# Optimization experiments

Hardware: AMD Instinct MI355X
Metric: run time of the kernel (lower is better)

The kernel has to match this reference:

```python
import jax, jax.numpy as jnp
import numpy as np

N_HEADS = 16

@jax.checkpoint
def feature_fn(x, neurons, weights):
    # x [B,S,D], neurons [N,D,R], weights [B,S,N] -> h [B,S,R]
    all_h = jnp.einsum('bsd,ndr->bsnr', x, neurons)
    return jnp.einsum('bsnr,bsn->bsr', all_h, weights)

@jax.checkpoint
def restore_fn(h, neurons, weights):
    # h [B,S,R], neurons [N,R,D], weights [B,S,N] -> out [B,S,D]
    all_out = jnp.einsum('bsr,nrd->bsnd', h, neurons)
    return jnp.einsum('bsnd,bsn->bsd', all_out, weights)


def setup_inputs() -> dict:
    key = jax.random.key(0)
    ks = jax.random.split(key, 12)
    B, S, D, R, N = 2, 2048, 1024, 128, 8
    inp = {
        'x': jax.random.normal(ks[0], (B, S, D), jnp.float32),
        'f_qk_neurons': jax.random.normal(ks[1], (N, D, R), jnp.float32) * 0.02,
        'f_v_neurons': jax.random.normal(ks[2], (N, D, R), jnp.float32) * 0.02,
        'r_qk_neurons': jax.random.normal(ks[3], (N, R, D), jnp.float32) * 0.02,
        'r_v_neurons': jax.random.normal(ks[4], (N, R, D), jnp.float32) * 0.02,
        'fqk_weights_Q': jax.random.uniform(ks[5], (B, S, N), jnp.float32),
        'fqk_weights_K': jax.random.uniform(ks[6], (B, S, N), jnp.float32),
        'fv_weights': jax.random.uniform(ks[7], (B, S, N), jnp.float32),
        'rqk_weights_Q': jax.random.uniform(ks[8], (B, S, N), jnp.float32),
        'rqk_weights_K': jax.random.uniform(ks[9], (B, S, N), jnp.float32),
        'rv_weights': jax.random.uniform(ks[10], (B, S, N), jnp.float32),
        'W_O': jax.random.normal(ks[11], (D, D), jnp.float32) * 0.02,
    }
    return inp


def reference(x, f_qk_neurons, f_v_neurons, r_qk_neurons, r_v_neurons,
              fqk_weights_Q, fqk_weights_K, fv_weights,
              rqk_weights_Q, rqk_weights_K, rv_weights, W_O):
    B, S, D = x.shape
    H = N_HEADS
    d_head = D // H
    # neuron-mixture feature projections (shared QK pool)
    h_q = feature_fn(x, f_qk_neurons, fqk_weights_Q)
    h_k = feature_fn(x, f_qk_neurons, fqk_weights_K)
    h_v = feature_fn(x, f_v_neurons, fv_weights)
    # neuron-mixture restore projections
    Q = restore_fn(h_q, r_qk_neurons, rqk_weights_Q)
    K = restore_fn(h_k, r_qk_neurons, rqk_weights_K)
    V = restore_fn(h_v, r_v_neurons, rv_weights)
    # split heads: [B,S,D] -> [B,H,S,d_head]
    Q = Q.reshape(B, S, H, d_head).transpose(0, 2, 1, 3)
    K = K.reshape(B, S, H, d_head).transpose(0, 2, 1, 3)
    V = V.reshape(B, S, H, d_head).transpose(0, 2, 1, 3)
    scale = jnp.sqrt(jnp.float32(d_head))
    scores = jnp.einsum('bhsd,bhtd->bhst', Q, K) / scale
    causal_mask = jnp.tril(jnp.ones((S, S), dtype=jnp.bool_))
    scores = jnp.where(causal_mask, scores, jnp.finfo(scores.dtype).min)
    attn = jax.nn.softmax(scores, axis=-1)
    attn_out = jnp.einsum('bhst,bhtd->bhsd', attn, V)
    attn_out = attn_out.transpose(0, 2, 1, 3).reshape(B, S, D)
    return attn_out @ W_O
```

## Files before the change

### kernel.cpp

```cpp
#include <hip/hip_runtime.h>
#include <stdint.h>

typedef __attribute__((ext_vector_type(8))) __bf16 bf16x8;
typedef __attribute__((ext_vector_type(4))) float f32x4;
typedef __attribute__((ext_vector_type(4))) unsigned short us4;
typedef __attribute__((ext_vector_type(8))) unsigned short us8v;

__device__ __forceinline__ unsigned short f2b(float f){
  unsigned int u = __builtin_bit_cast(unsigned int, f);
  unsigned int r = (u + 0x7fffu + ((u >> 16) & 1u)) >> 16;
  return (unsigned short)r;
}
__device__ __forceinline__ unsigned short f2b_fast(float f){
  unsigned int u = __builtin_bit_cast(unsigned int, f);
  return (unsigned short)((u + 0x8000u) >> 16);
}
__device__ __forceinline__ float b2f(unsigned short h){
  unsigned int u = ((unsigned int)h) << 16;
  return __builtin_bit_cast(float, u);
}

#define KDIM 1024

__global__ __launch_bounds__(256) void k_prep(
    const float* __restrict__ x,   unsigned short* __restrict__ Xbf,
    const float* __restrict__ fqk, unsigned short* __restrict__ FqkT,
    const float* __restrict__ fv,  unsigned short* __restrict__ FvT,
    const float* __restrict__ rqk, unsigned short* __restrict__ RqkT,
    const float* __restrict__ rv,  unsigned short* __restrict__ RvT,
    const float* __restrict__ wo,  unsigned short* __restrict__ WOT)
{
  __shared__ float tile[32][33];
  int blk = blockIdx.x;
  int tid = threadIdx.x;
  if (blk < 4096){
    int idx = blk * 256 + tid;
    float4 v = ((const float4*)x)[idx];
    us4 o; o.x = f2b(v.x); o.y = f2b(v.y); o.z = f2b(v.z); o.w = f2b(v.w);
    ((us4*)Xbf)[idx] = o;
    return;
  }
  int t = blk - 4096;
  int mid = t >> 10;
  int within = t & 1023;
  const float* src; unsigned short* dst;
  int b, R, C, tr, tc;
  if (mid < 2){
    src = mid == 0 ? fqk : fv;  dst = mid == 0 ? FqkT : FvT;
    R = 1024; C = 128;
    b = within >> 7; int tw = within & 127; tr = tw >> 2; tc = tw & 3;
  } else {
    src = mid == 2 ? rqk : (mid == 3 ? rv : wo);
    dst = mid == 2 ? RqkT : (mid == 3 ? RvT : WOT);
    R = 1024; C = 1024;
    b = 0; tr = within >> 5; tc = within & 31;
  }
  int r = tid >> 3, c0 = (tid & 7) * 4;
  size_t base = (size_t)b * R * C;
  float4 v = *(const float4*)&src[base + (size_t)(tr*32 + r) * C + tc*32 + c0];
  tile[r][c0+0] = v.x; tile[r][c0+1] = v.y; tile[r][c0+2] = v.z; tile[r][c0+3] = v.w;
  __syncthreads();
  us4 o;
  o.x = f2b(tile[c0+0][r]); o.y = f2b(tile[c0+1][r]);
  o.z = f2b(tile[c0+2][r]); o.w = f2b(tile[c0+3][r]);
  *(us4*)&dst[base + (size_t)(tc*32 + r) * R + tr*32 + c0] = o;
}

__global__ __launch_bounds__(256) void k_mix(const unsigned short* __restrict__ AH,
    const float* __restrict__ fwq, const float* __restrict__ fwk, const float* __restrict__ fwv,
    const float* __restrict__ rwq, const float* __restrict__ rwk, const float* __restrict__ rwv,
    unsigned short* __restrict__ gq, unsigned short* __restrict__ gk, unsigned short* __restrict__ gv){
  int tid = threadIdx.x;
  int lb = tid >> 5, rq = tid & 31;
  int bs = blockIdx.x * 8 + lb;
  const unsigned short* row = AH + (size_t)bs * 2048;
  float fq[8], fk[8], fv8[8], rqw[8], rkw[8], rvw[8];
  #pragma unroll
  for (int n = 0; n < 8; n++){
    fq[n] = fwq[bs*8+n]; fk[n] = fwk[bs*8+n]; fv8[n] = fwv[bs*8+n];
    rqw[n] = rwq[bs*8+n]; rkw[n] = rwk[bs*8+n]; rvw[n] = rwv[bs*8+n];
  }
  float hq[4] = {}, hk[4] = {}, hv[4] = {};
  #pragma unroll
  for (int n = 0; n < 8; n++){
    us4 a = *(const us4*)&row[n*128 + rq*4];
    us4 av = *(const us4*)&row[1024 + n*128 + rq*4];
    #pragma unroll
    for (int j = 0; j < 4; j++){
      float af = b2f(a[j]);
      hq[j] += af * fq[n]; hk[j] += af * fk[n];
      hv[j] += b2f(av[j]) * fv8[n];
    }
  }
  #pragma unroll
  for (int n = 0; n < 8; n++){
    us4 oq, ok, ov;
    #pragma unroll
    for (int j = 0; j < 4; j++){
      oq[j] = f2b(rqw[n] * hq[j]);
      ok[j] = f2b(rkw[n] * hk[j]);
      ov[j] = f2b(rvw[n] * hv[j]);
    }
    *(us4*)&gq[(size_t)bs*1024 + n*128 + rq*4] = oq;
    *(us4*)&gk[(size_t)bs*1024 + n*128 + rq*4] = ok;
    *(us4*)&gv[(size_t)bs*1024 + n*128 + rq*4] = ov;
  }
}


__device__ __forceinline__ void load_lds16(const void* g, void* l){
  __builtin_amdgcn_global_load_lds((const __attribute__((address_space(1))) unsigned int*)g,
                                   (__attribute__((address_space(3))) unsigned int*)l, 16, 0, 0);
}

template<int OUT_MODE, int OUT_MODE_J2, int BN, int ND, int NTILE>
__global__ __launch_bounds__(256) void k_gemm_bt3(
    const unsigned short* __restrict__ A0, const unsigned short* __restrict__ B0, void* __restrict__ C0,
    const unsigned short* __restrict__ A1, const unsigned short* __restrict__ B1, void* __restrict__ C1,
    const unsigned short* __restrict__ A2, const unsigned short* __restrict__ B2, void* __restrict__ C2)
{
  constexpr int STAGE_U16 = 2*128*32 + 2*BN*32;
  constexpr int SHSZ = (OUT_MODE_J2 == 3 && STAGE_U16 < 128*136) ? 128*136 : STAGE_U16;
  __shared__ __align__(16) unsigned short Sh[SHSZ];
  unsigned short (*Al)[128*32] = (unsigned short(*)[128*32])Sh;
  unsigned short (*Bl)[BN*32]  = (unsigned short(*)[BN*32])(Sh + 2*128*32);
  int nb8 = gridDim.x >> 3;
  int swz = (blockIdx.x & 7) * nb8 + (blockIdx.x >> 3);
  int job = swz / NTILE, bid = swz % NTILE;
  const unsigned short* A  = job == 0 ? A0 : (job == 1 ? A1 : A2);
  const unsigned short* Bt = job == 0 ? B0 : (job == 1 ? B1 : B2);
  void* C = job == 0 ? C0 : (job == 1 ? C1 : C2);
  constexpr int NBX = ND / BN;
  int bx = bid % NBX, by = bid / NBX;
  int m0 = by * 128, n0 = bx * BN;
  int tid = threadIdx.x, wid = tid >> 6, lane = tid & 63, l15 = lane & 15, g = lane >> 4;
  int wr = wid >> 1, wc = wid & 1;
  constexpr int WCN = BN / 2;
  constexpr int NACC = WCN / 16;

  auto stage = [&](int buf, int kt){
    #pragma unroll
    for (int i = 0; i < 2; i++){
      int c = i * 256 + tid;
      load_lds16(A + (size_t)(m0 + (c >> 2)) * KDIM + kt * 32 + (c & 3) * 8,
                 &Al[buf][(i * 256 + wid * 64) * 8]);
    }
    #pragma unroll
    for (int i = 0; i < BN/64; i++){
      int c = i * 256 + tid;
      load_lds16(Bt + (size_t)(n0 + (c >> 2)) * KDIM + kt * 32 + (c & 3) * 8,
                 &Bl[buf][(i * 256 + wid * 64) * 8]);
    }
  };

  f32x4 acc[4][NACC] = {};

  stage(0, 0);
  __syncthreads();
  int cur = 0;
  const int nk = KDIM / 32;
  for (int kt = 0; kt < nk; ++kt){
    if (kt + 1 < nk) stage(cur ^ 1, kt + 1);
    bf16x8 af[4], bfv[NACC];
    #pragma unroll
    for (int mi = 0; mi < 4; mi++)
      af[mi] = *(const bf16x8*)&Al[cur][(wr*64 + mi*16 + l15) * 32 + g * 8];
    #pragma unroll
    for (int ni = 0; ni < NACC; ni++)
      bfv[ni] = *(const bf16x8*)&Bl[cur][(wc*WCN + ni*16 + l15) * 32 + g * 8];
    #pragma unroll
    for (int mi = 0; mi < 4; mi++)
      #pragma unroll
      for (int ni = 0; ni < NACC; ni++)
        acc[mi][ni] = __builtin_amdgcn_mfma_f32_16x16x32_bf16(af[mi], bfv[ni], acc[mi][ni], 0, 0, 0);
    __syncthreads();
    cur ^= 1;
  }

  if constexpr (OUT_MODE == 0){
    #pragma unroll
    for (int mi = 0; mi < 4; mi++)
      #pragma unroll
      for (int reg = 0; reg < 4; reg++){
        int row = m0 + wr*64 + mi*16 + g*4 + reg;
        #pragma unroll
        for (int ni = 0; ni < NACC; ni++){
          int col = n0 + wc*WCN + ni*16 + l15;
          ((float*)C)[(size_t)row * ND + col] = acc[mi][ni][reg];
        }
      }
  } else {
    if (OUT_MODE_J2 == 3 && job == 2){
      unsigned short* Ct = Sh;
      #pragma unroll
      for (int mi = 0; mi < 4; mi++)
        #pragma unroll
        for (int reg = 0; reg < 4; reg++){
          int lrow = wr*64 + mi*16 + g*4 + reg;
          #pragma unroll
          for (int ni = 0; ni < NACC; ni++)
            Ct[(wc*WCN + ni*16 + l15)*136 + lrow] = f2b(acc[mi][ni][reg]);
        }
      __syncthreads();
      int bb = m0 >> 11, t128 = (m0 & 2047) >> 7, h0 = n0 >> 6;
      #pragma unroll
      for (int i = 0; i < 8; i++){
        int flat = i*256 + tid;
        int r = flat >> 4, c8 = (flat & 15) * 8;
        us8v v = *(const us8v*)&Ct[r*136 + c8];
        int h = r >> 6, dh = r & 63;
        int bh = bb*16 + h0 + h;
        *(us8v*)&((unsigned short*)C)[(((size_t)(bh*16 + t128))*64 + dh)*128 + c8] = v;
      }
    } else {
      unsigned short* Cl = Sh;
      #pragma unroll
      for (int mi = 0; mi < 4; mi++)
        #pragma unroll
        for (int reg = 0; reg < 4; reg++){
          int lrow = wr*64 + mi*16 + g*4 + reg;
          #pragma unroll
          for (int ni = 0; ni < NACC; ni++)
            Cl[lrow*BN + wc*WCN + ni*16 + l15] = f2b(acc[mi][ni][reg]);
        }
      __syncthreads();
      constexpr int VPT = (128*BN/8) / 256;
      #pragma unroll
      for (int i = 0; i < VPT; i++){
        int idx = i*256 + tid;
        int lrow = idx / (BN/8), c8 = (idx % (BN/8)) * 8;
        us8v v = *(const us8v*)&Cl[lrow*BN + c8];
        int row = m0 + lrow, col = n0 + c8;
        if (OUT_MODE == 1){
          *(us8v*)&((unsigned short*)C)[(size_t)row * ND + col] = v;
        } else {
          int b = row >> 11, s = row & 2047, h = col >> 6, dh = col & 63;
          *(us8v*)&((unsigned short*)C)[(((size_t)(b*16 + h)) * 2048 + s) * 64 + dh] = v;
        }
      }
    }
  }
}

#define PSTR 72
#define PBYTES 33792
__global__ __launch_bounds__(512) void k_attn(
    const unsigned short* __restrict__ Qp_, const unsigned short* __restrict__ Kp_,
    const unsigned short* __restrict__ Vt, unsigned short* __restrict__ AO,
    char* __restrict__ Pws)
{
  __shared__ unsigned short Klds[2][4096];
  __shared__ unsigned short Vlds[2][4096];
  __shared__ unsigned short Plds[8][32*PSTR];

  int xb = (blockIdx.x & 7) * 60 + (blockIdx.x >> 3);
  int bh = xb / 15;
  int slot = xb % 15;
  int qt, c;
  if (slot < 3){ qt = slot; c = 0; }
  else if (slot < 9){ int s = slot - 3; qt = 3 + (s >> 1); c = s & 1; }
  else { int s = slot - 9; qt = 6 + (s >= 3 ? 1 : 0); c = (s >= 3) ? s - 3 : s; }
  int nc = qt < 3 ? 1 : (qt < 6 ? 2 : 3);
  int b = bh >> 4, h = bh & 15;
  int q0 = qt * 256;
  int kv_lo = c * 768;
  int kv_hi = min((c + 1) * 768, q0 + 256);
  int niter = (kv_hi - kv_lo) >> 6;

  int tid = threadIdx.x, w = tid >> 6, lane = tid & 63, l15 = lane & 15, g = lane >> 4;
  const unsigned short* Qw = Qp_ + ((size_t)bh * 2048 + q0 + w*32) * 64;
  const unsigned short* Kb = Kp_ + (size_t)bh * 2048 * 64;
  const unsigned short* Vb = Vt + (size_t)bh * 16 * 64 * 128;
  unsigned short* Pw = &Plds[w][0];

  int srow = tid >> 3, sj = tid & 7;

  bf16x8 aq[2][2];
  #pragma unroll
  for (int m = 0; m < 2; m++)
    #pragma unroll
    for (int kk = 0; kk < 2; kk++)
      aq[m][kk] = *(const bf16x8*)(Qw + (m*16 + l15)*64 + kk*32 + g*8);

  const float cs = 0.125f;
  float l_run[2][4] = {};
  f32x4 acc_o[2][4] = {};

  us8v kA, vA, kB, vB;

  auto issue = [&](us8v& k0, us8v& v0, int kv0){
    k0 = *(const us8v*)(Kb + ((size_t)(kv0 + srow)) * 64 + sj*8);
    int t128 = kv0 >> 7, koff = kv0 & 64;
    v0 = *(const us8v*)(Vb + ((size_t)(t128*64 + srow)) * 128 + koff + sj*8);
  };
  auto put = [&](int buf, us8v k0, us8v v0){
    *(us8v*)&Klds[buf][(sj*64 + srow)*8] = k0;
    *(us8v*)&Vlds[buf][(sj*64 + srow)*8] = v0;
  };
  auto compute = [&](int buf, int kv0){
    f32x4 s4[2][4] = {};
    __builtin_amdgcn_s_setprio(1);
    #pragma unroll
    for (int ti = 0; ti < 4; ti++){
      #pragma unroll
      for (int kk = 0; kk < 2; kk++){
        bf16x8 kf = *(const bf16x8*)&Klds[buf][((kk*4 + g)*64 + ti*16 + l15)*8];
        s4[0][ti] = __builtin_amdgcn_mfma_f32_16x16x32_bf16(aq[0][kk], kf, s4[0][ti], 0, 0, 0);
        s4[1][ti] = __builtin_amdgcn_mfma_f32_16x16x32_bf16(aq[1][kk], kf, s4[1][ti], 0, 0, 0);
      }
    }
    __builtin_amdgcn_s_setprio(0);
    bool partial = (kv0 + 64 > q0);
    #pragma unroll
    for (int m = 0; m < 2; m++){
      #pragma unroll
      for (int reg = 0; reg < 4; reg++){
        int row = q0 + w*32 + m*16 + g*4 + reg;
        #pragma unroll
        for (int ti = 0; ti < 4; ti++){
          float x = s4[m][ti][reg] * cs;
          if (partial){
            int col = kv0 + ti*16 + l15;
            if (col > row) x = -1e30f;
          }
          float p = __expf(x);
          l_run[m][reg] += p;
          Pw[(m*16 + g*4 + reg)*PSTR + ((ti ^ g)*16) + l15] = f2b_fast(p);
        }
      }
    }
    bf16x8 pa[2][2];
    #pragma unroll
    for (int m = 0; m < 2; m++)
      #pragma unroll
      for (int cc = 0; cc < 2; cc++){
        int tiL = cc*2 + (g >> 1);
        int tiS = tiL ^ ((l15 >> 2) & 3);
        pa[m][cc] = *(const bf16x8*)&Pw[(m*16 + l15)*PSTR + tiS*16 + (g & 1)*8];
      }
    __builtin_amdgcn_s_setprio(1);
    #pragma unroll
    for (int ni = 0; ni < 4; ni++){
      #pragma unroll
      for (int cc = 0; cc < 2; cc++){
        bf16x8 vf = *(const bf16x8*)&Vlds[buf][((cc*4 + g)*64 + ni*16 + l15)*8];
        acc_o[0][ni] = __builtin_amdgcn_mfma_f32_16x16x32_bf16(pa[0][cc], vf, acc_o[0][ni], 0, 0, 0);
        acc_o[1][ni] = __builtin_amdgcn_mfma_f32_16x16x32_bf16(pa[1][cc], vf, acc_o[1][ni], 0, 0, 0);
      }
    }
    __builtin_amdgcn_s_setprio(0);
  };

  issue(kA, vA, kv_lo);
  put(0, kA, vA);
  __syncthreads();
  int it = 0, cur = 0;
  while (true){
    if (it + 1 < niter) issue(kB, vB, kv_lo + (it+1)*64);
    compute(cur, kv_lo + it*64);
    if (it + 1 < niter) put(cur ^ 1, kB, vB);
    __syncthreads();
    cur ^= 1; ++it;
    if (it >= niter) break;
    if (it + 1 < niter) issue(kA, vA, kv_lo + (it+1)*64);
    compute(cur, kv_lo + it*64);
    if (it + 1 < niter) put(cur ^ 1, kA, vA);
    __syncthreads();
    cur ^= 1; ++it;
    if (it >= niter) break;
  }

  #pragma unroll
  for (int m = 0; m < 2; m++)
    #pragma unroll
    for (int reg = 0; reg < 4; reg++){
      #pragma unroll
      for (int off = 1; off < 16; off <<= 1) l_run[m][reg] += __shfl_xor(l_run[m][reg], off);
    }

  if (nc == 1){
    #pragma unroll
    for (int m = 0; m < 2; m++)
      #pragma unroll
      for (int ni = 0; ni < 4; ni++)
        #pragma unroll
        for (int reg = 0; reg < 4; reg++){
          int row = q0 + w*32 + m*16 + g*4 + reg;
          int dh = ni*16 + l15;
          AO[((size_t)(b*2048 + row)) * 1024 + h*64 + dh] = f2b(acc_o[m][ni][reg] / l_run[m][reg]);
        }
  } else {
    int poff = (qt < 6) ? (qt - 3) * 2 : 6 + (qt - 6) * 3;
    char* P0 = Pws + ((size_t)(bh*12 + poff + c)) * PBYTES;
    unsigned short* Ob = (unsigned short*)P0;
    float* lb = (float*)(P0 + 32768);
    #pragma unroll
    for (int m = 0; m < 2; m++)
      #pragma unroll
      for (int ni = 0; ni < 4; ni++)
        #pragma unroll
        for (int reg = 0; reg < 4; reg++){
          int lrow = w*32 + m*16 + g*4 + reg;
          Ob[lrow*64 + ni*16 + l15] = f2b(acc_o[m][ni][reg]);
        }
    if (l15 == 0){
      #pragma unroll
      for (int m = 0; m < 2; m++)
        #pragma unroll
        for (int reg = 0; reg < 4; reg++){
          int lrow = w*32 + m*16 + g*4 + reg;
          lb[lrow] = l_run[m][reg];
        }
    }
  }
}

__global__ __launch_bounds__(256) void k_attn_reduce(const char* __restrict__ Pws,
                                                     unsigned short* __restrict__ AO){
  int blk = blockIdx.x;
  int rg = blk & 3, tmp = blk >> 2;
  int qtp = tmp % 5, bh = tmp / 5;
  int qt = qtp + 3;
  int b = bh >> 4, h = bh & 15;
  int nc = (qt < 6) ? 2 : 3;
  int poff = (qt < 6) ? (qt - 3) * 2 : 6 + (qt - 6) * 3;
  const char* base = Pws + ((size_t)(bh*12 + poff)) * PBYTES;
  int tid = threadIdx.x;
  int lrow = rg*64 + (tid >> 2);
  int d0 = (tid & 3) * 16;
  float o[16] = {};
  float l = 0.f;
  for (int cc = 0; cc < nc; ++cc){
    const unsigned short* Oc = (const unsigned short*)(base + (size_t)cc*PBYTES);
    const float* lc = (const float*)(base + (size_t)cc*PBYTES + 32768);
    us8v v0 = *(const us8v*)&Oc[lrow*64 + d0];
    us8v v1 = *(const us8v*)&Oc[lrow*64 + d0 + 8];
    #pragma unroll
    for (int j = 0; j < 8; j++){ o[j] += b2f(v0[j]); o[8+j] += b2f(v1[j]); }
    l += lc[lrow];
  }
  float inv = 1.f / l;
  us8v w0, w1;
  #pragma unroll
  for (int j = 0; j < 8; j++){ w0[j] = f2b(o[j]*inv); w1[j] = f2b(o[8+j]*inv); }
  size_t orow = ((size_t)(b*2048 + qt*256 + lrow)) * 1024 + h*64 + d0;
  *(us8v*)&AO[orow] = w0;
  *(us8v*)&AO[orow + 8] = w1;
}


extern "C" void kernel_launch(void* const* d_in, const int* in_sizes, int n_in,
                              void* d_out, int out_size, void* d_ws, size_t ws_size,
                              hipStream_t stream){
  const float* x    = (const float*)d_in[0];
  const float* fqk  = (const float*)d_in[1];
  const float* fv   = (const float*)d_in[2];
  const float* rqk  = (const float*)d_in[3];
  const float* rv   = (const float*)d_in[4];
  const float* fwQ  = (const float*)d_in[5];
  const float* fwK  = (const float*)d_in[6];
  const float* fwV  = (const float*)d_in[7];
  const float* rwQ  = (const float*)d_in[8];
  const float* rwK  = (const float*)d_in[9];
  const float* rwV  = (const float*)d_in[10];
  const float* wo   = (const float*)d_in[11];
  float* out = (float*)d_out;

  char* ws = (char*)d_ws;
  size_t off = 0;
  auto alloc = [&](size_t bytes)->void*{
    void* p = ws + off; off += (bytes + 255) & ~(size_t)255; return p;
  };
  unsigned short* FqkT = (unsigned short*)alloc(1024ull*1024*2);
  unsigned short* FvT  = (unsigned short*)alloc(1024ull*1024*2);
  unsigned short* RqkT = (unsigned short*)alloc(1024ull*1024*2);
  unsigned short* RvT  = (unsigned short*)alloc(1024ull*1024*2);
  unsigned short* WOT  = (unsigned short*)alloc(1024ull*1024*2);
  char* overlay = ws + off;
  unsigned short* Xbf  = (unsigned short*)alloc(4096ull*1024*2);
  unsigned short* AHc  = (unsigned short*)alloc(4096ull*2048*2);
  unsigned short* Gq   = (unsigned short*)alloc(4096ull*1024*2);
  unsigned short* Gk   = (unsigned short*)alloc(4096ull*1024*2);
  unsigned short* Gv   = (unsigned short*)alloc(4096ull*1024*2);
  unsigned short* Qp   = (unsigned short*)alloc(4096ull*1024*2);
  unsigned short* Kp   = (unsigned short*)alloc(4096ull*1024*2);
  unsigned short* Vtl  = (unsigned short*)alloc(32ull*16*64*128*2);
  unsigned short* AOm  = (unsigned short*)alloc(4096ull*1024*2);
  char* Pws = overlay;

  k_prep<<<9216, 256, 0, stream>>>(x, Xbf, fqk, FqkT, fv, FvT, rqk, RqkT, rv, RvT, wo, WOT);

  k_gemm_bt3<1,1,128,2048,512><<<512, 256, 0, stream>>>(Xbf, FqkT, AHc,
                                                        nullptr, nullptr, nullptr,
                                                        nullptr, nullptr, nullptr);
  k_mix<<<512, 256, 0, stream>>>(AHc, fwQ, fwK, fwV, rwQ, rwK, rwV, Gq, Gk, Gv);
  k_gemm_bt3<2,3,128,1024,256><<<768, 256, 0, stream>>>(Gq, RqkT, Qp, Gk, RqkT, Kp, Gv, RvT, Vtl);
  k_attn<<<480, 512, 0, stream>>>(Qp, Kp, Vtl, AOm, Pws);
  k_attn_reduce<<<640, 256, 0, stream>>>(Pws, AOm);
  k_gemm_bt3<0,0,64,1024,512><<<512, 256, 0, stream>>>(AOm, WOT, out,
                                                       nullptr, nullptr, nullptr,
                                                       nullptr, nullptr, nullptr);
}
```

Baseline: 172.8 us.

## Rebalance attention split-K work into 18 slots and merge Q/K restore GEMM

The causal attention partitioning changes from 15 slots with fixed 768-wide KV chunks to 18 table-driven slots per head with custom start and length, so per-block work is more even across 576 blocks. The reduce kernel is updated to match. K/V LDS is cut from double to single buffering, with an extra barrier per iteration, which lowers LDS use and may allow higher occupancy. The restore GEMM now runs Q and K as one stacked M=8192 job written into adjacent Qp/Kp buffers, which relies on Kp sitting directly after Qp in memory.

```diff
diff --git a/kernel.cpp b/kernel.cpp
--- a/kernel.cpp
+++ b/kernel.cpp
@@ -190,7 +190,7 @@
         }
       }
   } else {
-    if (OUT_MODE_J2 == 3 && job == 2){
+    if (OUT_MODE_J2 == 3 && job == 1){
       unsigned short* Ct = Sh;
       #pragma unroll
       for (int mi = 0; mi < 4; mi++)
@@ -234,8 +234,10 @@
         if (OUT_MODE == 1){
           *(us8v*)&((unsigned short*)C)[(size_t)row * ND + col] = v;
         } else {
-          int b = row >> 11, s = row & 2047, h = col >> 6, dh = col & 63;
-          *(us8v*)&((unsigned short*)C)[(((size_t)(b*16 + h)) * 2048 + s) * 64 + dh] = v;
+          int strm = row >> 12, tok = row & 4095;
+          int b = tok >> 11, s = tok & 2047, h = col >> 6, dh = col & 63;
+          *(us8v*)&((unsigned short*)C)[(size_t)strm*4194304 +
+                                        (((size_t)(b*16 + h)) * 2048 + s) * 64 + dh] = v;
         }
       }
     }
@@ -249,23 +251,22 @@
     const unsigned short* __restrict__ Vt, unsigned short* __restrict__ AO,
     char* __restrict__ Pws)
 {
-  __shared__ unsigned short Klds[2][4096];
-  __shared__ unsigned short Vlds[2][4096];
+  __shared__ unsigned short Klds[4096];
+  __shared__ unsigned short Vlds[4096];
   __shared__ unsigned short Plds[8][32*PSTR];
 
-  int xb = (blockIdx.x & 7) * 60 + (blockIdx.x >> 3);
-  int bh = xb / 15;
-  int slot = xb % 15;
-  int qt, c;
-  if (slot < 3){ qt = slot; c = 0; }
-  else if (slot < 9){ int s = slot - 3; qt = 3 + (s >> 1); c = s & 1; }
-  else { int s = slot - 9; qt = 6 + (s >= 3 ? 1 : 0); c = (s >= 3) ? s - 3 : s; }
-  int nc = qt < 3 ? 1 : (qt < 6 ? 2 : 3);
+  const unsigned int slot_pack[18] = {
+    4096u, 8193u, 6146u, 6346u, 8195u, 8459u, 10244u, 10572u, 8197u,
+    8461u, 8725u, 10246u, 9550u, 9846u, 8199u, 8463u, 8727u, 8991u };
+
+  int xb = (blockIdx.x & 7) * 72 + (blockIdx.x >> 3);
+  int bh = xb / 18;
+  int slot = xb % 18;
+  unsigned int sp = slot_pack[slot];
+  int qt = sp & 7, c = (sp >> 3) & 3, it0 = (sp >> 5) & 31, niter = sp >> 10;
   int b = bh >> 4, h = bh & 15;
   int q0 = qt * 256;
-  int kv_lo = c * 768;
-  int kv_hi = min((c + 1) * 768, q0 + 256);
-  int niter = (kv_hi - kv_lo) >> 6;
+  int kv_lo = it0 * 64;
 
   int tid = threadIdx.x, w = tid >> 6, lane = tid & 63, l15 = lane & 15, g = lane >> 4;
   const unsigned short* Qw = Qp_ + ((size_t)bh * 2048 + q0 + w*32) * 64;
@@ -293,18 +294,18 @@
     int t128 = kv0 >> 7, koff = kv0 & 64;
     v0 = *(const us8v*)(Vb + ((size_t)(t128*64 + srow)) * 128 + koff + sj*8);
   };
-  auto put = [&](int buf, us8v k0, us8v v0){
-    *(us8v*)&Klds[buf][(sj*64 + srow)*8] = k0;
-    *(us8v*)&Vlds[buf][(sj*64 + srow)*8] = v0;
+  auto put = [&](us8v k0, us8v v0){
+    *(us8v*)&Klds[(sj*64 + srow)*8] = k0;
+    *(us8v*)&Vlds[(sj*64 + srow)*8] = v0;
   };
-  auto compute = [&](int buf, int kv0){
+  auto compute = [&](int kv0){
     f32x4 s4[2][4] = {};
     __builtin_amdgcn_s_setprio(1);
     #pragma unroll
     for (int ti = 0; ti < 4; ti++){
       #pragma unroll
       for (int kk = 0; kk < 2; kk++){
-        bf16x8 kf = *(const bf16x8*)&Klds[buf][((kk*4 + g)*64 + ti*16 + l15)*8];
+        bf16x8 kf = *(const bf16x8*)&Klds[((kk*4 + g)*64 + ti*16 + l15)*8];
         s4[0][ti] = __builtin_amdgcn_mfma_f32_16x16x32_bf16(aq[0][kk], kf, s4[0][ti], 0, 0, 0);
         s4[1][ti] = __builtin_amdgcn_mfma_f32_16x16x32_bf16(aq[1][kk], kf, s4[1][ti], 0, 0, 0);
       }
@@ -343,7 +344,7 @@
     for (int ni = 0; ni < 4; ni++){
       #pragma unroll
       for (int cc = 0; cc < 2; cc++){
-        bf16x8 vf = *(const bf16x8*)&Vlds[buf][((cc*4 + g)*64 + ni*16 + l15)*8];
+        bf16x8 vf = *(const bf16x8*)&Vlds[((cc*4 + g)*64 + ni*16 + l15)*8];
         acc_o[0][ni] = __builtin_amdgcn_mfma_f32_16x16x32_bf16(pa[0][cc], vf, acc_o[0][ni], 0, 0, 0);
         acc_o[1][ni] = __builtin_amdgcn_mfma_f32_16x16x32_bf16(pa[1][cc], vf, acc_o[1][ni], 0, 0, 0);
       }
@@ -352,22 +353,27 @@
   };
 
   issue(kA, vA, kv_lo);
-  put(0, kA, vA);
+  put(kA, vA);
   __syncthreads();
-  int it = 0, cur = 0;
+  int it = 0;
   while (true){
-    if (it + 1 < niter) issue(kB, vB, kv_lo + (it+1)*64);
-    compute(cur, kv_lo + it*64);
-    if (it + 1 < niter) put(cur ^ 1, kB, vB);
+    bool more = (it + 1 < niter);
+    if (more) issue(kB, vB, kv_lo + (it+1)*64);
+    compute(kv_lo + it*64);
+    ++it;
+    if (!more) break;
     __syncthreads();
-    cur ^= 1; ++it;
-    if (it >= niter) break;
-    if (it + 1 < niter) issue(kA, vA, kv_lo + (it+1)*64);
-    compute(cur, kv_lo + it*64);
-    if (it + 1 < niter) put(cur ^ 1, kA, vA);
+    put(kB, vB);
     __syncthreads();
-    cur ^= 1; ++it;
-    if (it >= niter) break;
+
+    more = (it + 1 < niter);
+    if (more) issue(kA, vA, kv_lo + (it+1)*64);
+    compute(kv_lo + it*64);
+    ++it;
+    if (!more) break;
+    __syncthreads();
+    put(kA, vA);
+    __syncthreads();
   }
 
   #pragma unroll
@@ -378,7 +384,7 @@
       for (int off = 1; off < 16; off <<= 1) l_run[m][reg] += __shfl_xor(l_run[m][reg], off);
     }
 
-  if (nc == 1){
+  if (qt < 2){
     #pragma unroll
     for (int m = 0; m < 2; m++)
       #pragma unroll
@@ -390,8 +396,8 @@
           AO[((size_t)(b*2048 + row)) * 1024 + h*64 + dh] = f2b(acc_o[m][ni][reg] / l_run[m][reg]);
         }
   } else {
-    int poff = (qt < 6) ? (qt - 3) * 2 : 6 + (qt - 6) * 3;
-    char* P0 = Pws + ((size_t)(bh*12 + poff + c)) * PBYTES;
+    int poff = (13198368u >> ((qt - 2) * 4)) & 15;
+    char* P0 = Pws + ((size_t)(bh*16 + poff + c)) * PBYTES;
     unsigned short* Ob = (unsigned short*)P0;
     float* lb = (float*)(P0 + 32768);
     #pragma unroll
@@ -419,12 +425,12 @@
                                                      unsigned short* __restrict__ AO){
   int blk = blockIdx.x;
   int rg = blk & 3, tmp = blk >> 2;
-  int qtp = tmp % 5, bh = tmp / 5;
-  int qt = qtp + 3;
+  int qq = tmp % 6, bh = tmp / 6;
+  int qt = qq + 2;
   int b = bh >> 4, h = bh & 15;
-  int nc = (qt < 6) ? 2 : 3;
-  int poff = (qt < 6) ? (qt - 3) * 2 : 6 + (qt - 6) * 3;
-  const char* base = Pws + ((size_t)(bh*12 + poff)) * PBYTES;
+  int nc   = (4403746u  >> (qq * 4)) & 15;
+  int poff = (13198368u >> (qq * 4)) & 15;
+  const char* base = Pws + ((size_t)(bh*16 + poff)) * PBYTES;
   int tid = threadIdx.x;
   int lrow = rg*64 + (tid >> 2);
   int d0 = (tid & 3) * 16;
@@ -494,9 +500,10 @@
                                                         nullptr, nullptr, nullptr,
                                                         nullptr, nullptr, nullptr);
   k_mix<<<512, 256, 0, stream>>>(AHc, fwQ, fwK, fwV, rwQ, rwK, rwV, Gq, Gk, Gv);
-  k_gemm_bt3<2,3,128,1024,256><<<768, 256, 0, stream>>>(Gq, RqkT, Qp, Gk, RqkT, Kp, Gv, RvT, Vtl);
-  k_attn<<<480, 512, 0, stream>>>(Qp, Kp, Vtl, AOm, Pws);
-  k_attn_reduce<<<640, 256, 0, stream>>>(Pws, AOm);
+  k_gemm_bt3<2,3,128,1024,512><<<768, 256, 0, stream>>>(Gq, RqkT, Qp, Gv, RvT, Vtl,
+                                                        nullptr, nullptr, nullptr);
+  k_attn<<<576, 512, 0, stream>>>(Qp, Kp, Vtl, AOm, Pws);
+  k_attn_reduce<<<768, 256, 0, stream>>>(Pws, AOm);
   k_gemm_bt3<0,0,64,1024,512><<<512, 256, 0, stream>>>(AOm, WOT, out,
                                                        nullptr, nullptr, nullptr,
                                                        nullptr, nullptr, nullptr);
```

Result: slower. 176.3 us (+2.0%).
